# Performance work log

Hardware: AMD Instinct MI355X
Metric: run time of the kernel (lower is better)

## Reference

```python
import jax, jax.numpy as jnp
import numpy as np

L, C = 256, 20
BATCH = 1024


def _pairwise_mask(L, C, mask_type='pairwise'):
    # mask[l1, c1, l2, c2] nonzero iff positions interact (l2 - l1 >= 1, or == 1 for neighbor)
    ls = jnp.arange(L)
    d = ls[None, :] - ls[:, None]  # [L, L] = l2 - l1
    m = (d >= 1) if mask_type == 'pairwise' else (d == 1)
    return jnp.broadcast_to(m[:, None, :, None], (L, C, L, C)).astype(jnp.float32)


def setup_inputs() -> dict:
    key = jax.random.key(0)
    k1, k2, k3 = jax.random.split(key, 3)
    x_lc = jax.random.uniform(k1, (BATCH, L * C), dtype=jnp.float32)
    theta_0 = jnp.zeros((1,), dtype=jnp.float32)
    theta_lc = jax.random.normal(k2, (L, C), dtype=jnp.float32) / np.sqrt(L)
    theta_lclc = jax.random.normal(k3, (L, C, L, C), dtype=jnp.float32) / np.sqrt(L * L)
    return {"x_lc": x_lc, "theta_0": theta_0, "theta_lc": theta_lc, "theta_lclc": theta_lclc}


def reference(x_lc, theta_0, theta_lc, theta_lclc):
    Ld, Cd = theta_lc.shape
    mask = _pairwise_mask(Ld, Cd, 'pairwise')
    # additive term: sum_lc theta_lc * x_lc  -> [B, 1]
    lin = x_lc @ theta_lc.reshape(Ld * Cd)  # [B]
    # pairwise term: x^T (theta * mask) x, expressed as a masked GEMM instead of a
    # broadcasted [B, L, C, L, C] product
    Theta = (theta_lclc * mask).reshape(Ld * Cd, Ld * Cd)  # [LC, LC]
    xm = x_lc @ Theta  # [B, LC]
    quad = jnp.sum(xm * x_lc, axis=1)  # [B]
    phi = theta_0 + (lin + quad)[:, None]  # [B, 1]
    return phi
```

## Files before the change

### kernel.cpp

```cpp
#include <hip/hip_runtime.h>
#include <hip/hip_bf16.h>
#include <cstdint>
#include <cstddef>

#define LCN 5120
#define BN  1024
#define CN  20

typedef __attribute__((ext_vector_type(4))) float  floatx4;
typedef __attribute__((ext_vector_type(8))) short  shortx8;
typedef __attribute__((ext_vector_type(4))) unsigned short ushortx4;
typedef __attribute__((ext_vector_type(8))) unsigned short ushortx8;

static __device__ __forceinline__ unsigned short f2bf(float f) {
    __hip_bfloat16 h = __float2bfloat16(f);
    return *reinterpret_cast<unsigned short*>(&h);
}

static __device__ __forceinline__ void gload_lds16(const void* g, void* l) {
    __builtin_amdgcn_global_load_lds(
        (const __attribute__((address_space(1))) void*)g,
        (__attribute__((address_space(3))) void*)l,
        16, 0, 0);
}

__global__ __launch_bounds__(256) void k_prep(
    const float* __restrict__ th,
    const float* __restrict__ x,
    const float* __restrict__ th0,
    const float* __restrict__ thlc,
    unsigned short* __restrict__ Tb,
    unsigned short* __restrict__ Xb,
    float*          __restrict__ out)
{
    const int tid = threadIdx.x;
    if (blockIdx.x < LCN / 4) {
        const int w = tid >> 6, lane = tid & 63;
        const int i = blockIdx.x * 4 + w;
        const int lmin = ((i >> 8) << 8) / CN;
        const int js   = 1024 * ((CN * (lmin + 1)) / 1024);
        const int jmin = CN * (i / CN) + CN;
        const float* src = th + (size_t)i * LCN;
        unsigned short* dst = Tb + (size_t)i * LCN;
        for (int j = js + lane * 8; j < LCN; j += 512) {
            const floatx4 v0 = *reinterpret_cast<const floatx4*>(src + j);
            const floatx4 v1 = *reinterpret_cast<const floatx4*>(src + j + 4);
            ushortx8 o;
#pragma unroll
            for (int e = 0; e < 4; ++e) o[e]     = (j + e     >= jmin) ? f2bf(v0[e]) : (unsigned short)0;
#pragma unroll
            for (int e = 0; e < 4; ++e) o[4 + e] = (j + 4 + e >= jmin) ? f2bf(v1[e]) : (unsigned short)0;
            *reinterpret_cast<ushortx8*>(dst + j) = o;
        }
    } else {
        const int b = blockIdx.x - LCN / 4;
        const floatx4* xr = reinterpret_cast<const floatx4*>(x + (size_t)b * LCN);
        const floatx4* tr = reinterpret_cast<const floatx4*>(thlc);
        ushortx4* xw = reinterpret_cast<ushortx4*>(Xb + (size_t)b * LCN);
        float s = 0.0f;
        for (int k = tid; k < LCN / 4; k += 256) {
            const floatx4 a = xr[k], t2 = tr[k];
            s += a[0] * t2[0] + a[1] * t2[1] + a[2] * t2[2] + a[3] * t2[3];
            ushortx4 o;
#pragma unroll
            for (int e = 0; e < 4; ++e) o[e] = f2bf(a[e]);
            xw[k] = o;
        }
#pragma unroll
        for (int off = 32; off > 0; off >>= 1) s += __shfl_down(s, off, 64);
        __shared__ float ws4[4];
        if ((tid & 63) == 0) ws4[tid >> 6] = s;
        __syncthreads();
        if (tid == 0) out[b] = th0[0] + ws4[0] + ws4[1] + ws4[2] + ws4[3];
    }
}

__global__ __launch_bounds__(512, 2) void k_quad(
    const unsigned short* __restrict__ Xb,
    const unsigned short* __restrict__ Tb,
    float*                __restrict__ out)
{
    const int bid  = blockIdx.x;
    const int xcd  = bid & 7;
    const int slot = bid >> 3;
    const int m    = slot & 3;
    const int cl   = slot >> 2;
    int qc = cl * 8 + xcd;
    if (qc >= 60) return;

    int n = 0, cs = 0;
    for (int t = 0; t < 20; ++t) {
        const int lmin = (256 * t) / CN;
        const int c0   = (CN * (lmin + 1)) / 1024;
        const int cnt  = 5 - c0;
        if (qc < cnt) { n = t; cs = c0 + qc; break; }
        qc -= cnt;
    }
    const int b0 = m * 256;
    const int n0 = n * 256;
    const int k0 = cs * 1024;

    __shared__ unsigned short As[2 * 256 * 32];
    __shared__ unsigned short Bs[2 * 256 * 32];
    __shared__ float partial[256];

    const int tid  = threadIdx.x;
    const int lane = tid & 63;
    const int w    = tid >> 6;
    const int wm   = w & 1;
    const int wn   = w >> 1;
    const int lrow = lane & 15;
    const int kq   = lane >> 4;

    if (tid < 256) partial[tid] = 0.0f;

    floatx4 acc[8][4];
#pragma unroll
    for (int mt = 0; mt < 8; ++mt)
#pragma unroll
        for (int nt = 0; nt < 4; ++nt) acc[mt][nt] = (floatx4)0.0f;

    int aoff[8], boff[4];
#pragma unroll
    for (int mt = 0; mt < 8; ++mt) {
        const int row = wm * 128 + mt * 16 + lrow;
        aoff[mt] = row * 32 + (((kq + (row >> 1)) & 3) << 3);
    }
#pragma unroll
    for (int nt = 0; nt < 4; ++nt) {
        const int row = wn * 64 + nt * 16 + lrow;
        boff[nt] = row * 32 + (((kq + (row >> 1)) & 3) << 3);
    }

#define STAGE(buf, kc) do {                                                       \
    _Pragma("unroll")                                                             \
    for (int t = 0; t < 2; ++t) {                                                 \
        const int s    = t * 512 + tid;                                           \
        const int row  = s >> 2;                                                  \
        const int gseg = ((s & 3) - (row >> 1)) & 3;                              \
        char* la = (char*)As + (buf) * 16384 + (size_t)(t * 512 + w * 64) * 16;   \
        char* lb = (char*)Bs + (buf) * 16384 + (size_t)(t * 512 + w * 64) * 16;   \
        gload_lds16(Xb + (size_t)(b0 + row) * LCN + (kc) + gseg * 8, la);         \
        gload_lds16(Tb + (size_t)(n0 + row) * LCN + (kc) + gseg * 8, lb);         \
    }                                                                             \
} while (0)

    STAGE(0, k0);
#pragma unroll 2
    for (int kk = 0; kk < 32; ++kk) {
        const int cur = kk & 1;
        if (kk < 31) {
            STAGE(cur ^ 1, k0 + (kk + 1) * 32);
            asm volatile("s_waitcnt vmcnt(4)" ::: "memory");
        } else {
            asm volatile("s_waitcnt vmcnt(0)" ::: "memory");
        }
        __builtin_amdgcn_s_barrier();

        const unsigned short* Ab = As + cur * 8192;
        const unsigned short* Bb = Bs + cur * 8192;
        shortx8 bf4[4];
#pragma unroll
        for (int nt = 0; nt < 4; ++nt)
            bf4[nt] = *reinterpret_cast<const shortx8*>(Bb + boff[nt]);
        shortx8 af8[8];
#pragma unroll
        for (int mt = 0; mt < 8; ++mt)
            af8[mt] = *reinterpret_cast<const shortx8*>(Ab + aoff[mt]);
#pragma unroll
        for (int mt = 0; mt < 8; ++mt)
#pragma unroll
            for (int nt = 0; nt < 4; ++nt)
                acc[mt][nt] = __builtin_amdgcn_mfma_f32_16x16x32_bf16(af8[mt], bf4[nt], acc[mt][nt], 0, 0, 0);

        __builtin_amdgcn_s_barrier();
    }
#undef STAGE

#pragma unroll
    for (int mt = 0; mt < 8; ++mt) {
#pragma unroll
        for (int r = 0; r < 4; ++r) {
            const int b = b0 + wm * 128 + mt * 16 + kq * 4 + r;
            float s = 0.0f;
#pragma unroll
            for (int nt = 0; nt < 4; ++nt) {
                const int i = n0 + wn * 64 + nt * 16 + lrow;
                const __hip_bfloat16 hv = *reinterpret_cast<const __hip_bfloat16*>(&Xb[(size_t)b * LCN + i]);
                s += acc[mt][nt][r] * __bfloat162float(hv);
            }
            s += __shfl_xor(s, 1, 64);
            s += __shfl_xor(s, 2, 64);
            s += __shfl_xor(s, 4, 64);
            s += __shfl_xor(s, 8, 64);
            if (lrow == 0) atomicAdd(&partial[b - b0], s);
        }
    }
    __syncthreads();
    if (tid < 256) atomicAdd(&out[b0 + tid], partial[tid]);
}

extern "C" void kernel_launch(void* const* d_in, const int* in_sizes, int n_in,
                              void* d_out, int out_size, void* d_ws, size_t ws_size,
                              hipStream_t stream) {
    const float* x      = (const float*)d_in[0];
    const float* th0    = (const float*)d_in[1];
    const float* thlc   = (const float*)d_in[2];
    const float* thlclc = (const float*)d_in[3];
    float* out = (float*)d_out;

    unsigned short* Tb = (unsigned short*)d_ws;
    unsigned short* Xb = (unsigned short*)((char*)d_ws + (size_t)LCN * LCN * 2);

    k_prep<<<dim3(LCN / 4 + BN), 256, 0, stream>>>(thlclc, x, th0, thlc, Tb, Xb, out);

    k_quad<<<dim3(256), 512, 0, stream>>>(Xb, Tb, out);
}
```

Baseline: 213.3 us.

## Fuse theta bf16 conversion and masking into GEMM B-tile loading

The prep kernel no longer converts and masks the whole fp32 theta matrix into a bf16 workspace copy. The GEMM kernel now loads fp32 theta rows straight into registers, applies the triangular mask, converts to bf16 and writes the tile into LDS. A deeper software pipeline overlaps this register path with the async X loads and the MFMA work. This removes a full write and re-read of the bf16 theta, at the cost of more VGPR pressure, more manual vmcnt bookkeeping, and twice the global bytes for B inside the GEMM.

New measurement: 226.7 us. +6.3%, slower.

```diff
diff --git a/kernel.cpp b/kernel.cpp
--- a/kernel.cpp
+++ b/kernel.cpp
@@ -6,6 +6,7 @@
 #define LCN 5120
 #define BN  1024
 #define CN  20
+#define NT  32
 
 typedef __attribute__((ext_vector_type(4))) float  floatx4;
 typedef __attribute__((ext_vector_type(8))) short  shortx8;
@@ -25,59 +26,37 @@
 }
 
 __global__ __launch_bounds__(256) void k_prep(
-    const float* __restrict__ th,
     const float* __restrict__ x,
     const float* __restrict__ th0,
     const float* __restrict__ thlc,
-    unsigned short* __restrict__ Tb,
-    unsigned short* __restrict__ Xb,
+    unsigned short* __restrict__ Xg,
     float*          __restrict__ out)
 {
     const int tid = threadIdx.x;
-    if (blockIdx.x < LCN / 4) {
-        const int w = tid >> 6, lane = tid & 63;
-        const int i = blockIdx.x * 4 + w;
-        const int lmin = ((i >> 8) << 8) / CN;
-        const int js   = 1024 * ((CN * (lmin + 1)) / 1024);
-        const int jmin = CN * (i / CN) + CN;
-        const float* src = th + (size_t)i * LCN;
-        unsigned short* dst = Tb + (size_t)i * LCN;
-        for (int j = js + lane * 8; j < LCN; j += 512) {
-            const floatx4 v0 = *reinterpret_cast<const floatx4*>(src + j);
-            const floatx4 v1 = *reinterpret_cast<const floatx4*>(src + j + 4);
-            ushortx8 o;
-#pragma unroll
-            for (int e = 0; e < 4; ++e) o[e]     = (j + e     >= jmin) ? f2bf(v0[e]) : (unsigned short)0;
-#pragma unroll
-            for (int e = 0; e < 4; ++e) o[4 + e] = (j + 4 + e >= jmin) ? f2bf(v1[e]) : (unsigned short)0;
-            *reinterpret_cast<ushortx8*>(dst + j) = o;
-        }
-    } else {
-        const int b = blockIdx.x - LCN / 4;
-        const floatx4* xr = reinterpret_cast<const floatx4*>(x + (size_t)b * LCN);
-        const floatx4* tr = reinterpret_cast<const floatx4*>(thlc);
-        ushortx4* xw = reinterpret_cast<ushortx4*>(Xb + (size_t)b * LCN);
-        float s = 0.0f;
-        for (int k = tid; k < LCN / 4; k += 256) {
-            const floatx4 a = xr[k], t2 = tr[k];
-            s += a[0] * t2[0] + a[1] * t2[1] + a[2] * t2[2] + a[3] * t2[3];
-            ushortx4 o;
-#pragma unroll
-            for (int e = 0; e < 4; ++e) o[e] = f2bf(a[e]);
-            xw[k] = o;
-        }
-#pragma unroll
-        for (int off = 32; off > 0; off >>= 1) s += __shfl_down(s, off, 64);
-        __shared__ float ws4[4];
-        if ((tid & 63) == 0) ws4[tid >> 6] = s;
-        __syncthreads();
-        if (tid == 0) out[b] = th0[0] + ws4[0] + ws4[1] + ws4[2] + ws4[3];
-    }
+    const int b = blockIdx.x;
+    const floatx4* xr = reinterpret_cast<const floatx4*>(x + (size_t)b * LCN);
+    const floatx4* tr = reinterpret_cast<const floatx4*>(thlc);
+    ushortx4* xw = reinterpret_cast<ushortx4*>(Xg + (size_t)b * LCN);
+    float s = 0.0f;
+    for (int k = tid; k < LCN / 4; k += 256) {
+        const floatx4 a = xr[k], t2 = tr[k];
+        s += a[0] * t2[0] + a[1] * t2[1] + a[2] * t2[2] + a[3] * t2[3];
+        ushortx4 o;
+#pragma unroll
+        for (int e = 0; e < 4; ++e) o[e] = f2bf(a[e]);
+        xw[k] = o;
+    }
+#pragma unroll
+    for (int off = 32; off > 0; off >>= 1) s += __shfl_down(s, off, 64);
+    __shared__ float ws4[4];
+    if ((tid & 63) == 0) ws4[tid >> 6] = s;
+    __syncthreads();
+    if (tid == 0) out[b] = th0[0] + ws4[0] + ws4[1] + ws4[2] + ws4[3];
 }
 
 __global__ __launch_bounds__(512, 2) void k_quad(
-    const unsigned short* __restrict__ Xb,
-    const unsigned short* __restrict__ Tb,
+    const unsigned short* __restrict__ Xg,
+    const float*          __restrict__ th,
     float*                __restrict__ out)
 {
     const int bid  = blockIdx.x;
@@ -114,6 +93,16 @@
 
     if (tid < 256) partial[tid] = 0.0f;
 
+    const int br   = tid >> 1;
+    const int bp   = tid & 1;
+    const int bi   = n0 + br;
+    const int jmin = (bi / CN) * CN + CN;
+    const float* bsrc = th + (size_t)bi * LCN;
+    const int slot0 = ((2 * bp)     + (br >> 1)) & 3;
+    const int slot1 = ((2 * bp + 1) + (br >> 1)) & 3;
+    const int wadr0 = br * 32 + slot0 * 8;
+    const int wadr1 = br * 32 + slot1 * 8;
+
     floatx4 acc[8][4];
 #pragma unroll
     for (int mt = 0; mt < 8; ++mt)
@@ -132,50 +121,87 @@
         boff[nt] = row * 32 + (((kq + (row >> 1)) & 3) << 3);
     }
 
-#define STAGE(buf, kc) do {                                                       \
-    _Pragma("unroll")                                                             \
-    for (int t = 0; t < 2; ++t) {                                                 \
-        const int s    = t * 512 + tid;                                           \
-        const int row  = s >> 2;                                                  \
-        const int gseg = ((s & 3) - (row >> 1)) & 3;                              \
-        char* la = (char*)As + (buf) * 16384 + (size_t)(t * 512 + w * 64) * 16;   \
-        char* lb = (char*)Bs + (buf) * 16384 + (size_t)(t * 512 + w * 64) * 16;   \
-        gload_lds16(Xb + (size_t)(b0 + row) * LCN + (kc) + gseg * 8, la);         \
-        gload_lds16(Tb + (size_t)(n0 + row) * LCN + (kc) + gseg * 8, lb);         \
-    }                                                                             \
-} while (0)
-
-    STAGE(0, k0);
-#pragma unroll 2
-    for (int kk = 0; kk < 32; ++kk) {
-        const int cur = kk & 1;
-        if (kk < 31) {
-            STAGE(cur ^ 1, k0 + (kk + 1) * 32);
-            asm volatile("s_waitcnt vmcnt(4)" ::: "memory");
-        } else {
-            asm volatile("s_waitcnt vmcnt(0)" ::: "memory");
-        }
-        __builtin_amdgcn_s_barrier();
-
-        const unsigned short* Ab = As + cur * 8192;
-        const unsigned short* Bb = Bs + cur * 8192;
-        shortx8 bf4[4];
-#pragma unroll
-        for (int nt = 0; nt < 4; ++nt)
-            bf4[nt] = *reinterpret_cast<const shortx8*>(Bb + boff[nt]);
-        shortx8 af8[8];
-#pragma unroll
-        for (int mt = 0; mt < 8; ++mt)
-            af8[mt] = *reinterpret_cast<const shortx8*>(Ab + aoff[mt]);
-#pragma unroll
-        for (int mt = 0; mt < 8; ++mt)
-#pragma unroll
-            for (int nt = 0; nt < 4; ++nt)
-                acc[mt][nt] = __builtin_amdgcn_mfma_f32_16x16x32_bf16(af8[mt], bf4[nt], acc[mt][nt], 0, 0, 0);
-
-        __builtin_amdgcn_s_barrier();
-    }
-#undef STAGE
+    floatx4 S0a, S0b, S0c, S0d, S1a, S1b, S1c, S1d;
+
+#define ISSUE_B(S, kc) do {                                                   \
+    const float* p_ = bsrc + (kc) + bp * 16;                                  \
+    S##a = *reinterpret_cast<const floatx4*>(p_);                             \
+    S##b = *reinterpret_cast<const floatx4*>(p_ + 4);                         \
+    S##c = *reinterpret_cast<const floatx4*>(p_ + 8);                         \
+    S##d = *reinterpret_cast<const floatx4*>(p_ + 12);                        \
+} while (0)
+
+#define WRITEB(S, PARW, kcw) do {                                             \
+    const int j0_ = (kcw) + bp * 16;                                          \
+    ushortx8 o0_, o1_;                                                        \
+    _Pragma("unroll")                                                         \
+    for (int e = 0; e < 4; ++e) {                                             \
+        o0_[e]     = (j0_ + e      >= jmin) ? f2bf(S##a[e]) : (unsigned short)0; \
+        o0_[4 + e] = (j0_ + 4 + e  >= jmin) ? f2bf(S##b[e]) : (unsigned short)0; \
+        o1_[e]     = (j0_ + 8 + e  >= jmin) ? f2bf(S##c[e]) : (unsigned short)0; \
+        o1_[4 + e] = (j0_ + 12 + e >= jmin) ? f2bf(S##d[e]) : (unsigned short)0; \
+    }                                                                         \
+    *reinterpret_cast<ushortx8*>(&Bs[(PARW) * 8192 + wadr0]) = o0_;           \
+    *reinterpret_cast<ushortx8*>(&Bs[(PARW) * 8192 + wadr1]) = o1_;           \
+} while (0)
+
+#define ISSUE_A(PARA, kc) do {                                                \
+    _Pragma("unroll")                                                         \
+    for (int t_ = 0; t_ < 2; ++t_) {                                          \
+        const int s_   = t_ * 512 + tid;                                      \
+        const int row_ = s_ >> 2;                                             \
+        const int g_   = ((s_ & 3) - (row_ >> 1)) & 3;                        \
+        char* la_ = (char*)As + (PARA) * 16384 + (size_t)(t_ * 512 + w * 64) * 16; \
+        gload_lds16(Xg + (size_t)(b0 + row_) * LCN + (kc) + g_ * 8, la_);     \
+    }                                                                         \
+} while (0)
+
+    ISSUE_B(S1, k0);
+    ISSUE_A(0, k0);
+    asm volatile("s_waitcnt vmcnt(2)" ::: "memory");
+    WRITEB(S1, 0, k0);
+    ISSUE_B(S0, k0 + 32);
+    ISSUE_A(1, k0 + 32);
+    ISSUE_B(S1, k0 + 64);
+    asm volatile("s_waitcnt vmcnt(10)" ::: "memory");
+    asm volatile("s_waitcnt lgkmcnt(0)" ::: "memory");
+    __builtin_amdgcn_s_barrier();
+
+#define BODY(kk, PAR, S) do {                                                 \
+    shortx8 bfv[4], afv[8];                                                   \
+    _Pragma("unroll")                                                         \
+    for (int nt = 0; nt < 4; ++nt)                                            \
+        bfv[nt] = *reinterpret_cast<const shortx8*>(&Bs[(PAR) * 8192 + boff[nt]]); \
+    _Pragma("unroll")                                                         \
+    for (int mt = 0; mt < 8; ++mt)                                            \
+        afv[mt] = *reinterpret_cast<const shortx8*>(&As[(PAR) * 8192 + aoff[mt]]); \
+    asm volatile("s_waitcnt lgkmcnt(0)" ::: "memory");   \
+    __builtin_amdgcn_s_barrier();                        \
+    if ((kk) < NT - 2) { asm volatile("s_waitcnt vmcnt(6)" ::: "memory"); }   \
+    else               { asm volatile("s_waitcnt vmcnt(2)" ::: "memory"); }   \
+    if ((kk) + 1 < NT) WRITEB(S, (PAR) ^ 1, k0 + ((kk) + 1) * 32);            \
+    if ((kk) + 2 < NT) ISSUE_A(PAR, k0 + ((kk) + 2) * 32);                    \
+    if ((kk) + 3 < NT) ISSUE_B(S, k0 + ((kk) + 3) * 32);                      \
+    _Pragma("unroll")                                                         \
+    for (int mt = 0; mt < 8; ++mt)                                            \
+        _Pragma("unroll")                                                     \
+        for (int nt = 0; nt < 4; ++nt)                                        \
+            acc[mt][nt] = __builtin_amdgcn_mfma_f32_16x16x32_bf16(afv[mt], bfv[nt], acc[mt][nt], 0, 0, 0); \
+    if ((kk) < NT - 3)       { asm volatile("s_waitcnt vmcnt(10)" ::: "memory"); } \
+    else if ((kk) == NT - 3) { asm volatile("s_waitcnt vmcnt(6)"  ::: "memory"); } \
+    else                     { asm volatile("s_waitcnt vmcnt(0)"  ::: "memory"); } \
+    asm volatile("s_waitcnt lgkmcnt(0)" ::: "memory");   \
+    __builtin_amdgcn_s_barrier();                          \
+} while (0)
+
+    for (int kk = 0; kk < NT; kk += 2) {
+        BODY(kk, 0, S0);
+        BODY(kk + 1, 1, S1);
+    }
+#undef BODY
+#undef ISSUE_A
+#undef WRITEB
+#undef ISSUE_B
 
 #pragma unroll
     for (int mt = 0; mt < 8; ++mt) {
@@ -186,7 +212,7 @@
 #pragma unroll
             for (int nt = 0; nt < 4; ++nt) {
                 const int i = n0 + wn * 64 + nt * 16 + lrow;
-                const __hip_bfloat16 hv = *reinterpret_cast<const __hip_bfloat16*>(&Xb[(size_t)b * LCN + i]);
+                const __hip_bfloat16 hv = *reinterpret_cast<const __hip_bfloat16*>(&Xg[(size_t)b * LCN + i]);
                 s += acc[mt][nt][r] * __bfloat162float(hv);
             }
             s += __shfl_xor(s, 1, 64);
@@ -209,10 +235,9 @@
     const float* thlclc = (const float*)d_in[3];
     float* out = (float*)d_out;
 
-    unsigned short* Tb = (unsigned short*)d_ws;
-    unsigned short* Xb = (unsigned short*)((char*)d_ws + (size_t)LCN * LCN * 2);
-
-    k_prep<<<dim3(LCN / 4 + BN), 256, 0, stream>>>(thlclc, x, th0, thlc, Tb, Xb, out);
-
-    k_quad<<<dim3(256), 512, 0, stream>>>(Xb, Tb, out);
-}
+    unsigned short* Xb = (unsigned short*)d_ws;
+
+    k_prep<<<dim3(BN), 256, 0, stream>>>(x, th0, thlc, Xb, out);
+
+    k_quad<<<dim3(256), 512, 0, stream>>>(Xb, thlclc, out);
+}
```

## Deepen GEMM LDS pipeline to four-stage ring with one barrier per step

Applied to the files above, without the earlier changes.

Replaces the double-buffered LDS staging in the quadratic-form GEMM with a four-slot ring buffer that prefetches three K-steps ahead. The waitcnt is placed before a single barrier per iteration, removing the second barrier. MFMA issue is wrapped in s_setprio to favour the math wave. The cost is LDS growing to about 128KB per block, which rules out the two blocks per CU that launch_bounds requests; the grid is small enough that this likely matters little.

Result: no change. 212.9 us (-0.2%).

```diff
diff --git a/kernel.cpp b/kernel.cpp
--- a/kernel.cpp
+++ b/kernel.cpp
@@ -100,8 +100,8 @@
     const int n0 = n * 256;
     const int k0 = cs * 1024;
 
-    __shared__ unsigned short As[2 * 256 * 32];
-    __shared__ unsigned short Bs[2 * 256 * 32];
+    __shared__ unsigned short As[4 * 256 * 32];
+    __shared__ unsigned short Bs[4 * 256 * 32];
     __shared__ float partial[256];
 
     const int tid  = threadIdx.x;
@@ -145,36 +145,41 @@
     }                                                                             \
 } while (0)
 
+#define BODY(kk, PAR, VM) do {                                                     \
+    asm volatile("s_waitcnt vmcnt(" #VM ")" ::: "memory");                         \
+    __builtin_amdgcn_s_barrier();                                                  \
+    if ((kk) + 3 < 32) STAGE(((PAR) + 3) & 3, k0 + ((kk) + 3) * 32);               \
+    shortx8 bf4[4], af8[8];                                                        \
+    _Pragma("unroll")                                                              \
+    for (int nt = 0; nt < 4; ++nt)                                                 \
+        bf4[nt] = *reinterpret_cast<const shortx8*>(Bs + (PAR) * 8192 + boff[nt]); \
+    _Pragma("unroll")                                                              \
+    for (int mt = 0; mt < 8; ++mt)                                                 \
+        af8[mt] = *reinterpret_cast<const shortx8*>(As + (PAR) * 8192 + aoff[mt]); \
+    __builtin_amdgcn_s_setprio(1);                                                 \
+    _Pragma("unroll")                                                              \
+    for (int mt = 0; mt < 8; ++mt)                                                 \
+        _Pragma("unroll")                                                          \
+        for (int nt = 0; nt < 4; ++nt)                                             \
+            acc[mt][nt] = __builtin_amdgcn_mfma_f32_16x16x32_bf16(af8[mt], bf4[nt], acc[mt][nt], 0, 0, 0); \
+    __builtin_amdgcn_s_setprio(0);                                                 \
+} while (0)
+
     STAGE(0, k0);
-#pragma unroll 2
-    for (int kk = 0; kk < 32; ++kk) {
-        const int cur = kk & 1;
-        if (kk < 31) {
-            STAGE(cur ^ 1, k0 + (kk + 1) * 32);
-            asm volatile("s_waitcnt vmcnt(4)" ::: "memory");
-        } else {
-            asm volatile("s_waitcnt vmcnt(0)" ::: "memory");
-        }
-        __builtin_amdgcn_s_barrier();
-
-        const unsigned short* Ab = As + cur * 8192;
-        const unsigned short* Bb = Bs + cur * 8192;
-        shortx8 bf4[4];
-#pragma unroll
-        for (int nt = 0; nt < 4; ++nt)
-            bf4[nt] = *reinterpret_cast<const shortx8*>(Bb + boff[nt]);
-        shortx8 af8[8];
-#pragma unroll
-        for (int mt = 0; mt < 8; ++mt)
-            af8[mt] = *reinterpret_cast<const shortx8*>(Ab + aoff[mt]);
-#pragma unroll
-        for (int mt = 0; mt < 8; ++mt)
-#pragma unroll
-            for (int nt = 0; nt < 4; ++nt)
-                acc[mt][nt] = __builtin_amdgcn_mfma_f32_16x16x32_bf16(af8[mt], bf4[nt], acc[mt][nt], 0, 0, 0);
-
-        __builtin_amdgcn_s_barrier();
-    }
+    STAGE(1, k0 + 32);
+    STAGE(2, k0 + 64);
+
+    for (int kk = 0; kk < 28; kk += 4) {
+        BODY(kk + 0, 0, 8);
+        BODY(kk + 1, 1, 8);
+        BODY(kk + 2, 2, 8);
+        BODY(kk + 3, 3, 8);
+    }
+    BODY(28, 0, 8);
+    BODY(29, 1, 8);
+    BODY(30, 2, 4);
+    BODY(31, 3, 0);
+#undef BODY
 #undef STAGE
 
 #pragma unroll
```

## Double K-tile depth to 64 with one barrier per stage and MFMA priority

Applied to the files above, without the earlier changes.

The GEMM main loop now stages 64-wide K tiles instead of 32, halving the number of iterations and barriers. It uses a single barrier per iteration, issuing the next stage's loads right after the barrier. Global source pointers are precomputed and incremented, and the LDS layout uses an 8-way XOR-style swizzle. MFMA blocks are wrapped in s_setprio to favour compute waves. LDS use doubles to about 128KB per block, which may limit occupancy to one block per CU despite launch_bounds(512,2).

Result: no change. 217.4 us (+1.9%).

```diff
diff --git a/kernel.cpp b/kernel.cpp
--- a/kernel.cpp
+++ b/kernel.cpp
@@ -100,8 +100,8 @@
     const int n0 = n * 256;
     const int k0 = cs * 1024;
 
-    __shared__ unsigned short As[2 * 256 * 32];
-    __shared__ unsigned short Bs[2 * 256 * 32];
+    __shared__ unsigned short As[2 * 256 * 64];
+    __shared__ unsigned short Bs[2 * 256 * 64];
     __shared__ float partial[256];
 
     const int tid  = threadIdx.x;
@@ -120,62 +120,72 @@
 #pragma unroll
         for (int nt = 0; nt < 4; ++nt) acc[mt][nt] = (floatx4)0.0f;
 
-    int aoff[8], boff[4];
+    const int rbase = tid >> 3;
+    const int gseg  = ((tid & 7) - (rbase & 7)) & 7;
+    const unsigned short* aS[4];
+    const unsigned short* bS[4];
+#pragma unroll
+    for (int t = 0; t < 4; ++t) {
+        aS[t] = Xb + (size_t)(b0 + t * 64 + rbase) * LCN + k0 + gseg * 8;
+        bS[t] = Tb + (size_t)(n0 + t * 64 + rbase) * LCN + k0 + gseg * 8;
+    }
+
+    int aoff[8][2], boff[4][2];
 #pragma unroll
     for (int mt = 0; mt < 8; ++mt) {
         const int row = wm * 128 + mt * 16 + lrow;
-        aoff[mt] = row * 32 + (((kq + (row >> 1)) & 3) << 3);
+#pragma unroll
+        for (int ks = 0; ks < 2; ++ks)
+            aoff[mt][ks] = row * 64 + ((((ks << 2) | kq) + row) & 7) * 8;
     }
 #pragma unroll
     for (int nt = 0; nt < 4; ++nt) {
         const int row = wn * 64 + nt * 16 + lrow;
-        boff[nt] = row * 32 + (((kq + (row >> 1)) & 3) << 3);
-    }
-
-#define STAGE(buf, kc) do {                                                       \
+#pragma unroll
+        for (int ks = 0; ks < 2; ++ks)
+            boff[nt][ks] = row * 64 + ((((ks << 2) | kq) + row) & 7) * 8;
+    }
+
+#define STAGE64(cur) do {                                                         \
     _Pragma("unroll")                                                             \
-    for (int t = 0; t < 2; ++t) {                                                 \
-        const int s    = t * 512 + tid;                                           \
-        const int row  = s >> 2;                                                  \
-        const int gseg = ((s & 3) - (row >> 1)) & 3;                              \
-        char* la = (char*)As + (buf) * 16384 + (size_t)(t * 512 + w * 64) * 16;   \
-        char* lb = (char*)Bs + (buf) * 16384 + (size_t)(t * 512 + w * 64) * 16;   \
-        gload_lds16(Xb + (size_t)(b0 + row) * LCN + (kc) + gseg * 8, la);         \
-        gload_lds16(Tb + (size_t)(n0 + row) * LCN + (kc) + gseg * 8, lb);         \
+    for (int t = 0; t < 4; ++t) {                                                 \
+        char* la = (char*)As + (cur) * 32768 + (size_t)(t * 512 + w * 64) * 16;   \
+        char* lb = (char*)Bs + (cur) * 32768 + (size_t)(t * 512 + w * 64) * 16;   \
+        gload_lds16(aS[t], la);                                                   \
+        gload_lds16(bS[t], lb);                                                   \
+        aS[t] += 64; bS[t] += 64;                                                 \
     }                                                                             \
 } while (0)
 
-    STAGE(0, k0);
-#pragma unroll 2
-    for (int kk = 0; kk < 32; ++kk) {
-        const int cur = kk & 1;
-        if (kk < 31) {
-            STAGE(cur ^ 1, k0 + (kk + 1) * 32);
-            asm volatile("s_waitcnt vmcnt(4)" ::: "memory");
-        } else {
-            asm volatile("s_waitcnt vmcnt(0)" ::: "memory");
-        }
+    STAGE64(0);
+
+    for (int p = 0; p < 16; ++p) {
+        const int cur = p & 1;
+        asm volatile("s_waitcnt vmcnt(0)" ::: "memory");
         __builtin_amdgcn_s_barrier();
-
-        const unsigned short* Ab = As + cur * 8192;
-        const unsigned short* Bb = Bs + cur * 8192;
-        shortx8 bf4[4];
-#pragma unroll
-        for (int nt = 0; nt < 4; ++nt)
-            bf4[nt] = *reinterpret_cast<const shortx8*>(Bb + boff[nt]);
-        shortx8 af8[8];
-#pragma unroll
-        for (int mt = 0; mt < 8; ++mt)
-            af8[mt] = *reinterpret_cast<const shortx8*>(Ab + aoff[mt]);
-#pragma unroll
-        for (int mt = 0; mt < 8; ++mt)
+        if (p < 15) STAGE64(cur ^ 1);
+
+        const unsigned short* Ab = As + cur * 16384;
+        const unsigned short* Bb = Bs + cur * 16384;
+#pragma unroll
+        for (int ks = 0; ks < 2; ++ks) {
+            shortx8 bf4[4], af8[8];
 #pragma unroll
             for (int nt = 0; nt < 4; ++nt)
-                acc[mt][nt] = __builtin_amdgcn_mfma_f32_16x16x32_bf16(af8[mt], bf4[nt], acc[mt][nt], 0, 0, 0);
-
-        __builtin_amdgcn_s_barrier();
-    }
-#undef STAGE
+                bf4[nt] = *reinterpret_cast<const shortx8*>(Bb + boff[nt][ks]);
+#pragma unroll
+            for (int mt = 0; mt < 8; ++mt)
+                af8[mt] = *reinterpret_cast<const shortx8*>(Ab + aoff[mt][ks]);
+            __builtin_amdgcn_s_setprio(1);
+#pragma unroll
+            for (int mt = 0; mt < 8; ++mt)
+#pragma unroll
+                for (int nt = 0; nt < 4; ++nt)
+                    acc[mt][nt] = __builtin_amdgcn_mfma_f32_16x16x32_bf16(af8[mt], bf4[nt], acc[mt][nt], 0, 0, 0);
+            __builtin_amdgcn_s_setprio(0);
+        }
+    }
+#undef STAGE64
 
 #pragma unroll
     for (int mt = 0; mt < 8; ++mt) {
```
